# Kernel optimization log

Measured on AMD Instinct MI355X. Metric: run time of the kernel, lower is better.

Reference implementation:

```python
import jax, jax.numpy as jnp
import numpy as np

VOCAB, EMBED, NFEAT, T, HIDDEN, NCLASS, BATCH = 50000, 50, 3, 120, 300, 5, 1024
D_IN = NFEAT * EMBED  # 150


def setup_inputs() -> dict:
    key = jax.random.key(0)
    ks = jax.random.split(key, 5)
    s_in = 1.0 / np.sqrt(D_IN)
    s_h = 1.0 / np.sqrt(HIDDEN)
    return {
        "ids": jax.random.randint(ks[0], (BATCH, T, NFEAT), 0, VOCAB, dtype=jnp.int32),
        "embed": jax.random.normal(ks[1], (VOCAB, EMBED), dtype=jnp.float32),
        "Wx": jax.random.normal(ks[2], (D_IN, 4 * HIDDEN), dtype=jnp.float32) * s_in,
        "Wh": jax.random.normal(ks[3], (HIDDEN, 4 * HIDDEN), dtype=jnp.float32) * s_h,
        "b": jnp.zeros((4 * HIDDEN,), dtype=jnp.float32),
        "U": jax.random.normal(ks[4], (HIDDEN, NCLASS), dtype=jnp.float32) * s_h,
        "b2": jnp.zeros((NCLASS,), dtype=jnp.float32),
    }


def reference(ids, embed, Wx, Wh, b, U, b2):
    # Embedding lookup + concat windows: (B, T, 3) -> (B, T, 150)
    x = embed[ids].reshape(ids.shape[0], T, D_IN)
    # Precompute input contribution for all timesteps: (B, T, 4H)
    xz = jnp.einsum("btd,dg->btg", x, Wx) + b
    xz = jnp.transpose(xz, (1, 0, 2))  # (T, B, 4H)

    def step(carry, xz_t):
        c, h = carry
        z = xz_t + h @ Wh  # (B, 4H)
        i, f, g, o = jnp.split(z, 4, axis=-1)
        i = jax.nn.sigmoid(i)
        f = jax.nn.sigmoid(f)
        o = jax.nn.sigmoid(o)
        g = jnp.tanh(g)
        c = f * c + i * g
        h = o * jnp.tanh(c)
        # dropout at inference (keep_prob=1) is identity
        y = h @ U + b2  # (B, C)
        return (c, h), y

    B = ids.shape[0]
    init = (jnp.zeros((B, HIDDEN), x.dtype), jnp.zeros((B, HIDDEN), x.dtype))
    _, ys = jax.lax.scan(step, init, xz)  # ys: (T, B, C)
    return jnp.transpose(ys, (1, 0, 2))  # (B, T, C)
```

## Files before the change

### kernel.cpp

```cpp
#include <hip/hip_runtime.h>


#define BATCH 1024
#define TT    120
#define HID   300
#define KX    160
#define KH    320
#define SL    64
#define HSL   60
#define NCOL  1280
#define GH    5
#define GB    32
#define BS    32
#define XST   168
#define FSTR  32
#define NSLOT 3
#define NB    256
#define NREL  (GH * 4)

typedef __attribute__((ext_vector_type(8))) short bf16x8;
typedef __attribute__((ext_vector_type(4))) float f32x4;

__device__ __forceinline__ unsigned short f2b(float f) {
  union { float f; unsigned u; } v; v.f = f;
  unsigned r = v.u + 0x7fffu + ((v.u >> 16) & 1u);
  return (unsigned short)(r >> 16);
}
__device__ __forceinline__ float sigm(float x) {
  return __builtin_amdgcn_rcpf(1.f + __expf(-x));
}
__device__ __forceinline__ float tanhf_(float x) {
  return 2.f * __builtin_amdgcn_rcpf(1.f + __expf(-2.f * x)) - 1.f;
}

__global__ void k_reorder_wh(const float* __restrict__ W, unsigned short* __restrict__ Wp) {
  int tid = blockIdx.x * 256 + threadIdx.x;
  if (tid >= KH * NCOL) return;
  int c = tid % NCOL, k = tid / NCOL;
  int js = k >> 6, v0 = k & 63;
  int j = c >> 8, r = c & 255, g = r >> 6, u0 = r & 63;
  float val = 0.f;
  if (v0 < HSL && u0 < HSL) val = W[(js * HSL + v0) * 1200 + g * 300 + j * HSL + u0];
  Wp[((k >> 3) * NCOL + c) * 8 + (k & 7)] = f2b(val);
}

__global__ void k_reorder_wx(const float* __restrict__ W, unsigned short* __restrict__ Wp) {
  int tid = blockIdx.x * 256 + threadIdx.x;
  if (tid >= KX * NCOL) return;
  int c = tid % NCOL, k = tid / NCOL;
  int j = c >> 8, r = c & 255, g = r >> 6, u0 = r & 63;
  float val = 0.f;
  if (k < 150 && u0 < HSL) val = W[k * 1200 + g * 300 + j * HSL + u0];
  Wp[((k >> 3) * NCOL + c) * 8 + (k & 7)] = f2b(val);
}

__global__ void k_reorder_b(const float* __restrict__ b, float* __restrict__ bp) {
  int c = blockIdx.x * 256 + threadIdx.x;
  if (c >= NCOL) return;
  int j = c >> 8, r = c & 255, g = r >> 6, u0 = r & 63;
  bp[c] = (u0 < HSL) ? b[g * 300 + j * HSL + u0] : 0.f;
}

__global__ void k_reorder_u(const float* __restrict__ U, unsigned short* __restrict__ Up) {
  int tid = blockIdx.x * 256 + threadIdx.x;
  if (tid >= KH * 16) return;
  int n = tid % 16, k = tid / 16;
  int js = k >> 6, v0 = k & 63;
  float v = (v0 < HSL && n < 5) ? U[(js * HSL + v0) * 5 + n] : 0.f;
  Up[((k >> 3) * 16 + n) * 8 + (k & 7)] = f2b(v);
}

__launch_bounds__(256, 1)
__attribute__((amdgpu_waves_per_eu(1, 1)))
__global__ void k_lstm(const int* __restrict__ ids, const float* __restrict__ embed,
                       const unsigned short* __restrict__ Wp,
                       const unsigned short* __restrict__ Wxp,
                       const float* __restrict__ bp,
                       const unsigned short* __restrict__ Up,
                       unsigned short* __restrict__ hbuf,
                       int* __restrict__ flags,
                       int* __restrict__ xcd_cnt,
                       const float* __restrict__ b2,
                       float* __restrict__ out) {
  __shared__ __align__(16) unsigned short x_lds[2][BS * XST];
  __shared__ char lds_pad[61440];
  __shared__ int role[2];

  const int tid = threadIdx.x;
  if (tid == 0) {
    ((volatile char*)lds_pad)[0] = 0;
    int xcd = __builtin_amdgcn_s_getreg(63508) & 7;
    int rank = atomicAdd(&xcd_cnt[xcd], 1);
    role[0] = xcd; role[1] = rank;
  }
  __syncthreads();
  const int xcd = role[0], rank = role[1];
  if (rank >= GH * 4) return;
  const int bg = xcd * 4 + rank / GH;
  const int j  = rank % GH;

  const int lane = tid & 63, w = tid >> 6;
  const int l15 = lane & 15, l4 = lane >> 4;

  if (tid < BS) {
#pragma unroll
    for (int bq = 0; bq < 2; ++bq)
      for (int e = 150; e < XST; ++e) x_lds[bq][tid * XST + e] = 0;
  }

  const int colb = j * 256 + w * 16 + l15;

  bf16x8 bh[10][4], bx[5][4];
#pragma unroll
  for (int kk = 0; kk < 10; ++kk)
#pragma unroll
    for (int g = 0; g < 4; ++g)
      bh[kk][g] = *(const bf16x8*)(Wp + ((kk * 4 + l4) * NCOL + colb + g * 64) * 8);
#pragma unroll
  for (int kk = 0; kk < 5; ++kk)
#pragma unroll
    for (int g = 0; g < 4; ++g)
      bx[kk][g] = *(const bf16x8*)(Wxp + ((kk * 4 + l4) * NCOL + colb + g * 64) * 8);

  float bias[4];
#pragma unroll
  for (int g = 0; g < 4; ++g) bias[g] = bp[colb + g * 64];
  const float b2v = (l15 < 5) ? b2[l15] : 0.f;

  int xrow = 0, koff = 0, nf2 = 0, f = 0;
  const bool gth = (tid < 192);
  if (gth) {
    xrow = tid / 6; int half = tid % 6; f = half >> 1; int hh = half & 1;
    nf2 = hh ? 12 : 13;
    koff = f * 50 + (hh ? 26 : 0);
  }
  const long idbase = (long)(bg * BS + xrow) * TT * 3 + f;
  const int  eoff   = (koff - f * 50);

  if (gth) {
    int id0 = ids[idbase + 0 * 3];
    const float* src = embed + (long)id0 * 50 + eoff;
    unsigned short* dst = &x_lds[0][xrow * XST + koff];
#pragma unroll
    for (int e = 0; e < 13; ++e)
      if (e < nf2) {
        float2 v = *(const float2*)(src + 2 * e);
        *(unsigned*)(dst + 2 * e) = (unsigned)f2b(v.x) | ((unsigned)f2b(v.y) << 16);
      }
  }
  __syncthreads();

  f32x4 acc[4][2];
  float cst[2][4];
#pragma unroll
  for (int g = 0; g < 4; ++g)
#pragma unroll
    for (int mt = 0; mt < 2; ++mt) acc[g][mt] = {0.f, 0.f, 0.f, 0.f};
#pragma unroll
  for (int mt = 0; mt < 2; ++mt)
#pragma unroll
    for (int r = 0; r < 4; ++r) cst[mt][r] = 0.f;

  {
    const unsigned short* xb = &x_lds[0][l15 * XST + l4 * 8];
#pragma unroll
    for (int kk = 0; kk < 5; ++kk) {
      bf16x8 a0 = *(const bf16x8*)(xb + kk * 32);
      bf16x8 a1 = *(const bf16x8*)(xb + 16 * XST + kk * 32);
#pragma unroll
      for (int g = 0; g < 4; ++g) {
        acc[g][0] = __builtin_amdgcn_mfma_f32_16x16x32_bf16(a0, bx[kk][g], acc[g][0], 0, 0, 0);
        acc[g][1] = __builtin_amdgcn_mfma_f32_16x16x32_bf16(a1, bx[kk][g], acc[g][1], 0, 0, 0);
      }
    }
  }

  float2 xv[13];
  int idv = 0;
  if (gth) {
    int id1 = ids[idbase + 1 * 3];
    const float* src = embed + (long)id1 * 50 + eoff;
#pragma unroll
    for (int e = 0; e < 13; ++e)
      if (e < nf2) xv[e] = *(const float2*)(src + 2 * e);
    idv = ids[idbase + 2 * 3];
  }

  bf16x8 va0[10], va1[10];

  for (int t = 0; t < TT; ++t) {
    if (t > 0) {
      const int* fp = flags + ((t - 1) * GB + bg) * FSTR;
      int it = 0;
      while (__hip_atomic_load(fp, __ATOMIC_RELAXED, __HIP_MEMORY_SCOPE_AGENT) < NREL) {
        if (++it > 300000) break;
      }
      asm volatile("buffer_inv\n\ts_waitcnt vmcnt(0)" ::: "memory");

      const unsigned short* ar =
          hbuf + ((t - 1) % NSLOT) * (BATCH * KH) + (bg * BS + l15) * KH + l4 * 8;
#pragma unroll
      for (int kk = 0; kk < 10; ++kk) {
        va0[kk] = *(const bf16x8*)(ar + kk * 32);
        va1[kk] = *(const bf16x8*)(ar + 16 * KH + kk * 32);
      }
#pragma unroll
      for (int kk = 0; kk < 10; ++kk) {
#pragma unroll
        for (int g = 0; g < 4; ++g) {
          acc[g][0] = __builtin_amdgcn_mfma_f32_16x16x32_bf16(va0[kk], bh[kk][g], acc[g][0], 0, 0, 0);
          acc[g][1] = __builtin_amdgcn_mfma_f32_16x16x32_bf16(va1[kk], bh[kk][g], acc[g][1], 0, 0, 0);
        }
      }
    }

    unsigned short* hdst = hbuf + (t % NSLOT) * (BATCH * KH);
#pragma unroll
    for (int mt = 0; mt < 2; ++mt) {
#pragma unroll
      for (int r = 0; r < 4; ++r) {
        float zi = acc[0][mt][r] + bias[0];
        float zf = acc[1][mt][r] + bias[1];
        float zg = acc[2][mt][r] + bias[2];
        float zo = acc[3][mt][r] + bias[3];
        float gi = sigm(zi), gf = sigm(zf), go = sigm(zo), gg = tanhf_(zg);
        float c = gf * cst[mt][r] + gi * gg;
        cst[mt][r] = c;
        float h = go * tanhf_(c);
        unsigned v = f2b(h);
        unsigned p1 = v | ((unsigned)__shfl_xor((int)v, 1) << 16);
        unsigned long long p2 = (unsigned long long)p1 |
            ((unsigned long long)(unsigned)__shfl_xor((int)p1, 2) << 32);
        if ((l15 & 3) == 0) {
          int row = bg * BS + mt * 16 + l4 * 4 + r;
          *(unsigned long long*)(hdst + row * KH + j * SL + w * 16 + l15) = p2;
        }
      }
      acc[0][mt] = {0.f, 0.f, 0.f, 0.f};
      acc[1][mt] = {0.f, 0.f, 0.f, 0.f};
      acc[2][mt] = {0.f, 0.f, 0.f, 0.f};
      acc[3][mt] = {0.f, 0.f, 0.f, 0.f};
    }

    asm volatile("s_waitcnt vmcnt(0)" ::: "memory");
    if ((tid & 63) == 0)
      __hip_atomic_fetch_add(flags + (t * GB + bg) * FSTR, 1, __ATOMIC_RELAXED,
                             __HIP_MEMORY_SCOPE_AGENT);

    if (t > 0 && j == (t - 1) % GH) {
      if (w == 2) {
        f32x4 ay = {0.f, 0.f, 0.f, 0.f};
#pragma unroll
        for (int kk = 0; kk < 10; ++kk) {
          bf16x8 u = *(const bf16x8*)(Up + ((kk * 4 + l4) * 16 + l15) * 8);
          ay = __builtin_amdgcn_mfma_f32_16x16x32_bf16(va0[kk], u, ay, 0, 0, 0);
        }
        if (l15 < 5)
#pragma unroll
          for (int q = 0; q < 4; ++q)
            out[((bg * BS + l4 * 4 + q) * TT + (t - 1)) * 5 + l15] = ay[q] + b2v;
      } else if (w == 3) {
        f32x4 ay = {0.f, 0.f, 0.f, 0.f};
#pragma unroll
        for (int kk = 0; kk < 10; ++kk) {
          bf16x8 u = *(const bf16x8*)(Up + ((kk * 4 + l4) * 16 + l15) * 8);
          ay = __builtin_amdgcn_mfma_f32_16x16x32_bf16(va1[kk], u, ay, 0, 0, 0);
        }
        if (l15 < 5)
#pragma unroll
          for (int q = 0; q < 4; ++q)
            out[((bg * BS + 16 + l4 * 4 + q) * TT + (t - 1)) * 5 + l15] = ay[q] + b2v;
      }
    }

    if (t + 1 < TT) {
      if (gth) {
        unsigned short* dst = &x_lds[(t + 1) & 1][xrow * XST + koff];
#pragma unroll
        for (int e = 0; e < 13; ++e)
          if (e < nf2)
            *(unsigned*)(dst + 2 * e) = (unsigned)f2b(xv[e].x) | ((unsigned)f2b(xv[e].y) << 16);
      }
      __syncthreads();
      const unsigned short* xb = &x_lds[(t + 1) & 1][l15 * XST + l4 * 8];
#pragma unroll
      for (int kk = 0; kk < 5; ++kk) {
        bf16x8 a0 = *(const bf16x8*)(xb + kk * 32);
        bf16x8 a1 = *(const bf16x8*)(xb + 16 * XST + kk * 32);
#pragma unroll
        for (int g = 0; g < 4; ++g) {
          acc[g][0] = __builtin_amdgcn_mfma_f32_16x16x32_bf16(a0, bx[kk][g], acc[g][0], 0, 0, 0);
          acc[g][1] = __builtin_amdgcn_mfma_f32_16x16x32_bf16(a1, bx[kk][g], acc[g][1], 0, 0, 0);
        }
      }
      if (gth && t + 2 < TT) {
        const float* src = embed + (long)idv * 50 + eoff;
#pragma unroll
        for (int e = 0; e < 13; ++e)
          if (e < nf2) xv[e] = *(const float2*)(src + 2 * e);
        if (t + 3 < TT) idv = ids[idbase + (long)(t + 3) * 3];
      }
    }
  }

  if (j == (TT - 1) % GH) {
    const int* fp = flags + ((TT - 1) * GB + bg) * FSTR;
    int it = 0;
    while (__hip_atomic_load(fp, __ATOMIC_RELAXED, __HIP_MEMORY_SCOPE_AGENT) < NREL) {
      if (++it > 300000) break;
    }
    asm volatile("buffer_inv\n\ts_waitcnt vmcnt(0)" ::: "memory");
    const unsigned short* ar =
        hbuf + ((TT - 1) % NSLOT) * (BATCH * KH) + (bg * BS + l15) * KH + l4 * 8;
#pragma unroll
    for (int kk = 0; kk < 10; ++kk) {
      va0[kk] = *(const bf16x8*)(ar + kk * 32);
      va1[kk] = *(const bf16x8*)(ar + 16 * KH + kk * 32);
    }
    if (w == 2) {
      f32x4 ay = {0.f, 0.f, 0.f, 0.f};
#pragma unroll
      for (int kk = 0; kk < 10; ++kk) {
        bf16x8 u = *(const bf16x8*)(Up + ((kk * 4 + l4) * 16 + l15) * 8);
        ay = __builtin_amdgcn_mfma_f32_16x16x32_bf16(va0[kk], u, ay, 0, 0, 0);
      }
      if (l15 < 5)
#pragma unroll
        for (int q = 0; q < 4; ++q)
          out[((bg * BS + l4 * 4 + q) * TT + (TT - 1)) * 5 + l15] = ay[q] + b2v;
    } else if (w == 3) {
      f32x4 ay = {0.f, 0.f, 0.f, 0.f};
#pragma unroll
      for (int kk = 0; kk < 10; ++kk) {
        bf16x8 u = *(const bf16x8*)(Up + ((kk * 4 + l4) * 16 + l15) * 8);
        ay = __builtin_amdgcn_mfma_f32_16x16x32_bf16(va1[kk], u, ay, 0, 0, 0);
      }
      if (l15 < 5)
#pragma unroll
        for (int q = 0; q < 4; ++q)
          out[((bg * BS + 16 + l4 * 4 + q) * TT + (TT - 1)) * 5 + l15] = ay[q] + b2v;
    }
  }
}

extern "C" void kernel_launch(void* const* d_in, const int* in_sizes, int n_in,
                              void* d_out, int out_size, void* d_ws, size_t ws_size,
                              hipStream_t stream) {
  const int*   ids   = (const int*)d_in[0];
  const float* embed = (const float*)d_in[1];
  const float* Wx    = (const float*)d_in[2];
  const float* Wh    = (const float*)d_in[3];
  const float* b     = (const float*)d_in[4];
  const float* U     = (const float*)d_in[5];
  const float* b2    = (const float*)d_in[6];
  float* out = (float*)d_out;

  char* ws = (char*)d_ws;
  size_t off = 0;
  unsigned short* Wp   = (unsigned short*)(ws + off); off += (size_t)KH * NCOL * 2;
  unsigned short* Wxp  = (unsigned short*)(ws + off); off += (size_t)KX * NCOL * 2;
  float*          bp   = (float*)(ws + off);          off += (size_t)NCOL * 4;
  unsigned short* Up   = (unsigned short*)(ws + off); off += (size_t)KH * 16 * 2;
  unsigned short* hbuf = (unsigned short*)(ws + off); off += (size_t)NSLOT * BATCH * KH * 2;
  int*            flags= (int*)(ws + off);            off += (size_t)TT * GB * FSTR * 4;
  int*            xcd_cnt = (int*)(ws + off);         off += 8 * 4;
  if (ws_size < off) return;

  hipMemsetAsync(flags, 0, TT * GB * FSTR * 4 + 8 * 4, stream);
  k_reorder_wh<<<(KH * NCOL + 255) / 256, 256, 0, stream>>>(Wh, Wp);
  k_reorder_wx<<<(KX * NCOL + 255) / 256, 256, 0, stream>>>(Wx, Wxp);
  k_reorder_b<<<(NCOL + 255) / 256, 256, 0, stream>>>(b, bp);
  k_reorder_u<<<(KH * 16 + 255) / 256, 256, 0, stream>>>(U, Up);

  k_lstm<<<dim3(NB), dim3(256), 0, stream>>>(ids, embed, Wp, Wxp, bp, Up,
                                             hbuf, flags, xcd_cnt, b2, out);
}
```

Before: 711.8 us.

## Keep B weights in AGPRs via inline MFMA, single-lane spin, kernel flag init

MFMA calls become inline asm that takes the B operand from accumulator registers, so the resident weight fragments can sit in AGPRs and free VGPRs. The flag spin-wait now runs only on lane 0 of each wave instead of all 64 lanes, which cuts polling traffic. The memset is replaced by a small init kernel using atomic stores, and the waves_per_eu attribute is dropped. Risks: forcing operands into AGPRs can add copies if the compiler keeps them in VGPRs, and the inline asm hides MFMA hazards from the scheduler.

```diff
diff --git a/kernel.cpp b/kernel.cpp
--- a/kernel.cpp
+++ b/kernel.cpp
@@ -32,6 +32,9 @@
 __device__ __forceinline__ float tanhf_(float x) {
   return 2.f * __builtin_amdgcn_rcpf(1.f + __expf(-2.f * x)) - 1.f;
 }
+__device__ __forceinline__ void mfma_bA(bf16x8 a, const bf16x8& b, f32x4& c) {
+  asm("v_mfma_f32_16x16x32_bf16 %0, %1, %2, %0" : "+v"(c) : "v"(a), "a"(b));
+}
 
 __global__ void k_reorder_wh(const float* __restrict__ W, unsigned short* __restrict__ Wp) {
   int tid = blockIdx.x * 256 + threadIdx.x;
@@ -70,8 +73,15 @@
   Up[((k >> 3) * 16 + n) * 8 + (k & 7)] = f2b(v);
 }
 
+__global__ void k_init(int* __restrict__ flags, int n, int* __restrict__ xcd_cnt) {
+  int i = blockIdx.x * 256 + threadIdx.x;
+  if (i < n)
+    __hip_atomic_store(flags + i, 0, __ATOMIC_RELAXED, __HIP_MEMORY_SCOPE_AGENT);
+  if (i < 8)
+    __hip_atomic_store(xcd_cnt + i, 0, __ATOMIC_RELAXED, __HIP_MEMORY_SCOPE_AGENT);
+}
+
 __launch_bounds__(256, 1)
-__attribute__((amdgpu_waves_per_eu(1, 1)))
 __global__ void k_lstm(const int* __restrict__ ids, const float* __restrict__ embed,
                        const unsigned short* __restrict__ Wp,
                        const unsigned short* __restrict__ Wxp,
@@ -169,8 +179,8 @@
       bf16x8 a1 = *(const bf16x8*)(xb + 16 * XST + kk * 32);
 #pragma unroll
       for (int g = 0; g < 4; ++g) {
-        acc[g][0] = __builtin_amdgcn_mfma_f32_16x16x32_bf16(a0, bx[kk][g], acc[g][0], 0, 0, 0);
-        acc[g][1] = __builtin_amdgcn_mfma_f32_16x16x32_bf16(a1, bx[kk][g], acc[g][1], 0, 0, 0);
+        mfma_bA(a0, bx[kk][g], acc[g][0]);
+        mfma_bA(a1, bx[kk][g], acc[g][1]);
       }
     }
   }
@@ -190,10 +200,12 @@
 
   for (int t = 0; t < TT; ++t) {
     if (t > 0) {
-      const int* fp = flags + ((t - 1) * GB + bg) * FSTR;
-      int it = 0;
-      while (__hip_atomic_load(fp, __ATOMIC_RELAXED, __HIP_MEMORY_SCOPE_AGENT) < NREL) {
-        if (++it > 300000) break;
+      if (lane == 0) {
+        const int* fp = flags + ((t - 1) * GB + bg) * FSTR;
+        int it = 0;
+        while (__hip_atomic_load(fp, __ATOMIC_RELAXED, __HIP_MEMORY_SCOPE_AGENT) < NREL) {
+          if (++it > 500000) break;
+        }
       }
       asm volatile("buffer_inv\n\ts_waitcnt vmcnt(0)" ::: "memory");
 
@@ -208,8 +220,8 @@
       for (int kk = 0; kk < 10; ++kk) {
 #pragma unroll
         for (int g = 0; g < 4; ++g) {
-          acc[g][0] = __builtin_amdgcn_mfma_f32_16x16x32_bf16(va0[kk], bh[kk][g], acc[g][0], 0, 0, 0);
-          acc[g][1] = __builtin_amdgcn_mfma_f32_16x16x32_bf16(va1[kk], bh[kk][g], acc[g][1], 0, 0, 0);
+          mfma_bA(va0[kk], bh[kk][g], acc[g][0]);
+          mfma_bA(va1[kk], bh[kk][g], acc[g][1]);
         }
       }
     }
@@ -243,7 +255,7 @@
     }
 
     asm volatile("s_waitcnt vmcnt(0)" ::: "memory");
-    if ((tid & 63) == 0)
+    if (lane == 0)
       __hip_atomic_fetch_add(flags + (t * GB + bg) * FSTR, 1, __ATOMIC_RELAXED,
                              __HIP_MEMORY_SCOPE_AGENT);
 
@@ -289,8 +301,8 @@
         bf16x8 a1 = *(const bf16x8*)(xb + 16 * XST + kk * 32);
 #pragma unroll
         for (int g = 0; g < 4; ++g) {
-          acc[g][0] = __builtin_amdgcn_mfma_f32_16x16x32_bf16(a0, bx[kk][g], acc[g][0], 0, 0, 0);
-          acc[g][1] = __builtin_amdgcn_mfma_f32_16x16x32_bf16(a1, bx[kk][g], acc[g][1], 0, 0, 0);
+          mfma_bA(a0, bx[kk][g], acc[g][0]);
+          mfma_bA(a1, bx[kk][g], acc[g][1]);
         }
       }
       if (gth && t + 2 < TT) {
@@ -304,10 +316,12 @@
   }
 
   if (j == (TT - 1) % GH) {
-    const int* fp = flags + ((TT - 1) * GB + bg) * FSTR;
-    int it = 0;
-    while (__hip_atomic_load(fp, __ATOMIC_RELAXED, __HIP_MEMORY_SCOPE_AGENT) < NREL) {
-      if (++it > 300000) break;
+    if (lane == 0) {
+      const int* fp = flags + ((TT - 1) * GB + bg) * FSTR;
+      int it = 0;
+      while (__hip_atomic_load(fp, __ATOMIC_RELAXED, __HIP_MEMORY_SCOPE_AGENT) < NREL) {
+        if (++it > 500000) break;
+      }
     }
     asm volatile("buffer_inv\n\ts_waitcnt vmcnt(0)" ::: "memory");
     const unsigned short* ar =
@@ -366,7 +380,7 @@
   int*            xcd_cnt = (int*)(ws + off);         off += 8 * 4;
   if (ws_size < off) return;
 
-  hipMemsetAsync(flags, 0, TT * GB * FSTR * 4 + 8 * 4, stream);
+  k_init<<<(TT * GB * FSTR + 255) / 256, 256, 0, stream>>>(flags, TT * GB * FSTR, xcd_cnt);
   k_reorder_wh<<<(KH * NCOL + 255) / 256, 256, 0, stream>>>(Wh, Wp);
   k_reorder_wx<<<(KX * NCOL + 255) / 256, 256, 0, stream>>>(Wx, Wxp);
   k_reorder_b<<<(NCOL + 255) / 256, 256, 0, stream>>>(b, bp);
```

Measured after the change: 671.9 us, median of 2. 1.06x faster.
